# Kernel optimization log

Hardware: AMD Instinct MI355X
Metric: run time of the kernel (lower is better)

Reference implementation:

```python
import jax, jax.numpy as jnp
import numpy as np

CONF_THRES = 0.4
IOU_THRES = 0.45
MAX_WH = 4096.0   # class offset for non-agnostic NMS (torch code: max_wh)
K_PRE = 1024      # candidates kept for the O(K^2) NMS stage (<= max_nms=30000)
MAX_DET = 300     # max detections per image (torch default)
B, N, NC = 16, 25200, 80


def xywh2xyxy(x):
    xy, wh = x[..., :2], x[..., 2:4]
    return jnp.concatenate([xy - wh * 0.5, xy + wh * 0.5], axis=-1)


def box_iou(a, b):
    # a: [K,4], b: [K,4] in xyxy
    area_a = (a[:, 2] - a[:, 0]) * (a[:, 3] - a[:, 1])
    area_b = (b[:, 2] - b[:, 0]) * (b[:, 3] - b[:, 1])
    lt = jnp.maximum(a[:, None, :2], b[None, :, :2])
    rb = jnp.minimum(a[:, None, 2:], b[None, :, 2:])
    inter = jnp.clip(rb - lt, 0.0, None).prod(-1)
    return inter / (area_a[:, None] + area_b[None, :] - inter + 1e-7)


def _nms_single(pred, conf_logit, logit, head):
    # pred [N,85] (decoded, sigmoided), conf_logit [N,5] raw, logit [N,80] raw, head [N]
    xc = pred[:, 4] > CONF_THRES                      # objectness gate
    obj_sig = jax.nn.sigmoid(conf_logit[:, 4:5])      # [N,1]
    log_sig = jax.nn.sigmoid(logit) * obj_sig         # sel_prob == 'objclass'
    cls_scores = pred[:, 5:] * pred[:, 4:5]           # x[:,5:] *= x[:,4:5]
    box = xywh2xyxy(pred[:, :4])                      # [N,4]
    conf = cls_scores.max(axis=1)                     # best class conf
    j = cls_scores.argmax(axis=1).astype(pred.dtype)  # best class id
    valid = xc & (conf > CONF_THRES)
    score = jnp.where(valid, conf, 0.0)
    # top-K candidates (sorted descending) -> fixed-shape NMS
    top_s, top_i = jax.lax.top_k(score, K_PRE)
    valid_k = top_s > 0.0
    boxes_k = box[top_i] + j[top_i, None] * MAX_WH    # per-class box offset (agnostic=False)
    iou = box_iou(boxes_k, boxes_k)                   # [K,K]
    idx = jnp.arange(K_PRE)

    def body(i, keep):
        sup = (iou[i] > IOU_THRES) & (idx > i) & keep[i]
        return keep & ~sup

    keep = jax.lax.fori_loop(0, K_PRE, body, valid_k)
    final_score = jnp.where(keep, top_s, 0.0)
    _, sel = jax.lax.top_k(final_score, MAX_DET)      # first MAX_DET survivors
    gi = top_i[sel]
    m = (final_score[sel] > 0.0).astype(pred.dtype)[:, None]  # validity mask
    det = jnp.concatenate([box[gi], conf[gi, None], j[gi, None]], axis=1)  # [300,6] xyxy,conf,cls
    # pack: det(6) | class logits*obj(80) | obj_conf(1) | classHead(1) | valid(1) -> [300,89]
    return jnp.concatenate(
        [det * m, log_sig[gi] * m, obj_sig[gi] * m, head[gi, None] * m, m], axis=1)


def setup_inputs() -> dict:
    key = jax.random.key(0)
    k1, k2, k3, k4, k5, k6 = jax.random.split(key, 6)
    xy = jax.random.uniform(k1, (B, N, 2), jnp.float32) * 640.0
    wh = 2.0 + jax.random.uniform(k2, (B, N, 2), jnp.float32) * 198.0
    objcls = jax.random.uniform(k3, (B, N, 1 + NC), jnp.float32)
    prediction = jnp.concatenate([xy, wh, objcls], axis=-1)       # [B,N,85]
    pred_conf_logits = jax.random.normal(k4, (B, N, 5), jnp.float32)
    logits = jax.random.normal(k5, (B, N, NC), jnp.float32)
    class_head = jax.random.randint(k6, (B, N), 0, 3).astype(jnp.float32)
    return {"prediction": prediction, "pred_conf_logits": pred_conf_logits,
            "logits": logits, "class_head": class_head}


def reference(prediction, pred_conf_logits, logits, class_head):
    return jax.vmap(_nms_single)(prediction, pred_conf_logits, logits, class_head)
```

## Files before the change

kernel.cpp:

```cpp
#include <hip/hip_runtime.h>
#include <math.h>

#define BATCH 16
#define NN 25200
#define NCLS 80
#define K_PRE 1024
#define MAX_DET 300
#define CONF_T 0.4f
#define IOU_T 0.45f
#define TBIAS 0x3E000000u
#define RROWS 128
#define STHREADS 512
#define CAND_STRIDE 50400

__global__ void __launch_bounds__(STHREADS) score_kernel(
    const float* __restrict__ pred, unsigned long long* __restrict__ keys,
    unsigned* __restrict__ ghist) {
    __shared__ float srow[RROWS * 85];
    __shared__ unsigned lh[1024];

    const int tile = blockIdx.x, b = blockIdx.y, tid = threadIdx.x;
    const int row0 = tile * RROWS;
    int nrows = NN - row0;
    if (nrows > RROWS) nrows = RROWS;

    const float4* g4 = (const float4*)(pred + ((size_t)b * NN + row0) * 85);
    float4* l4 = (float4*)srow;
    const int nf4 = (nrows * 85) >> 2;
    for (int i = tid; i < nf4; i += STHREADS) l4[i] = g4[i];
    lh[tid] = 0u;
    lh[tid + STHREADS] = 0u;
    __syncthreads();

    const int r = tid >> 2, sub = tid & 3;
    float best = 0.0f;
    int bc = sub * 20;
    float obj = 0.0f;
    if (r < nrows) {
        obj = srow[r * 85 + 4];
        if (obj > CONF_T) {
            const float* cp = &srow[r * 85 + 5 + sub * 20];
#pragma unroll
            for (int i = 0; i < 20; ++i) {
                float v = cp[i] * obj;
                if (v > best) { best = v; bc = sub * 20 + i; }
            }
        }
    }
#pragma unroll
    for (int d = 1; d < 4; d <<= 1) {
        float ov = __shfl_xor(best, d);
        int oc = __shfl_xor(bc, d);
        if (ov > best || (ov == best && oc < bc)) { best = ov; bc = oc; }
    }
    if (r < nrows && sub == 0) {
        unsigned t = (obj > CONF_T && best > CONF_T)
                         ? (__float_as_uint(best) - TBIAS) : 0u;
        int n = row0 + r;
        keys[(size_t)b * NN + n] =
            ((unsigned long long)t << 22) |
            ((unsigned long long)(unsigned)(NN - 1 - n) << 7) | (unsigned)bc;
        if (t) atomicAdd(&lh[t >> 15], 1u);
    }
    __syncthreads();
    for (int i = tid; i < 1024; i += STHREADS) {
        unsigned v = lh[i];
        if (v) atomicAdd(&ghist[b * 1024 + i], v);
    }
}

__global__ void __launch_bounds__(1024) topk_kernel(
    const unsigned long long* __restrict__ keys,
    const unsigned* __restrict__ ghist, const float* __restrict__ pred,
    float* __restrict__ ws_f) {
    __shared__ unsigned sA[1024], sB[1024];
    __shared__ unsigned long long skeys[2048];
    __shared__ unsigned sel_d0, sel_cnt;

    const int b = blockIdx.x, tid = threadIdx.x;
    const unsigned long long* bk = keys + (size_t)b * NN;

    unsigned* src = sA;
    unsigned* dst = sB;
    src[tid] = ghist[b * 1024 + tid];
    __syncthreads();
    for (int off = 1; off < 1024; off <<= 1) {
        dst[tid] = src[tid] + ((tid + off < 1024) ? src[tid + off] : 0u);
        __syncthreads();
        unsigned* t2 = src; src = dst; dst = t2;
    }
    unsigned total = src[0];
    unsigned K = total < 1024u ? total : 1024u;
    if (tid == 0) { sel_d0 = 0u; sel_cnt = 0u; }
    skeys[tid] = 0ull;
    skeys[tid + 1024] = 0ull;
    __syncthreads();
    if (total) {
        unsigned geq = src[tid];
        unsigned gt = (tid < 1023) ? src[tid + 1] : 0u;
        if (gt < K && K <= geq) sel_d0 = (unsigned)tid;
    }
    __syncthreads();
    const unsigned d0 = sel_d0;

    for (int base = 0; base < 25600; base += 1024) {
        int i = base + tid;
        if (i < NN) {
            unsigned long long key = bk[i];
            unsigned t = (unsigned)(key >> 22);
            if (t && (t >> 15) >= d0) {
                unsigned p = atomicAdd(&sel_cnt, 1u);
                if (p < 2048u) skeys[p] = key;
            }
        }
    }
    __syncthreads();

    for (unsigned k2 = 2; k2 <= 2048; k2 <<= 1) {
        for (unsigned j = k2 >> 1; j > 0; j >>= 1) {
            unsigned i = ((tid & ~(j - 1)) << 1) | (tid & (j - 1));
            unsigned ixj = i | j;
            unsigned long long a = skeys[i], c = skeys[ixj];
            bool desc = ((i & k2) == 0u);
            if (desc ? (a < c) : (a > c)) { skeys[i] = c; skeys[ixj] = a; }
            __syncthreads();
        }
    }

    unsigned long long key = skeys[tid];
    unsigned t = (unsigned)(key >> 22);
    int n = NN - 1 - (int)((key >> 7) & 32767u);
    float* cbase = ws_f + (size_t)b * CAND_STRIDE;
    float* cx0 = cbase;
    float* cy0 = cbase + 1024;
    float* cx1 = cbase + 2048;
    float* cy1 = cbase + 3072;
    float* carea = cbase + 4096;
    float* cscore = cbase + 5120;
    int* ccls = (int*)(cbase + 6144);
    int* cgi = (int*)(cbase + 7168);
    int* keep = (int*)(cbase + 8192);
    keep[tid] = 0;
    cgi[tid] = n;
    if (t == 0u) {
        ccls[tid] = 255;
    } else {
        const float* row = pred + ((size_t)b * NN + n) * 85;
        float x = row[0], y = row[1], w = row[2], h = row[3];
        float bx0 = x - w * 0.5f, by0 = y - h * 0.5f;
        float bx1 = x + w * 0.5f, by1 = y + h * 0.5f;
        cx0[tid] = bx0; cy0[tid] = by0; cx1[tid] = bx1; cy1[tid] = by1;
        carea[tid] = (bx1 - bx0) * (by1 - by0);
        cscore[tid] = __uint_as_float(t + TBIAS);
        ccls[tid] = (int)(key & 127u);
    }
}

__global__ void __launch_bounds__(64) nms_kernel(float* __restrict__ ws_f) {
    __shared__ int mlist[K_PRE];
    __shared__ float bx0[K_PRE], by0[K_PRE], bx1[K_PRE], by1[K_PRE],
        bar[K_PRE];
    __shared__ unsigned char kf[K_PRE];

    const int b = blockIdx.x / NCLS, c = blockIdx.x % NCLS;
    const int lane = threadIdx.x;
    float* cbase = ws_f + (size_t)b * CAND_STRIDE;
    const float* cx0 = cbase;
    const float* cy0 = cbase + 1024;
    const float* cx1 = cbase + 2048;
    const float* cy1 = cbase + 3072;
    const float* carea = cbase + 4096;
    const int* ccls = (const int*)(cbase + 6144);
    int* keep = (int*)(cbase + 8192);

    int m = 0;
    for (int w = 0; w < K_PRE / 64; ++w) {
        int i = w * 64 + lane;
        bool my = (ccls[i] == c);
        unsigned long long bal = __ballot(my);
        if (my) {
            int pos = __popcll(bal & ((1ull << lane) - 1ull));
            mlist[m + pos] = i;
        }
        m += __popcll(bal);
    }
    for (int j = lane; j < m; j += 64) {
        int i = mlist[j];
        bx0[j] = cx0[i]; by0[j] = cy0[i];
        bx1[j] = cx1[i]; by1[j] = cy1[i];
        bar[j] = carea[i];
        kf[j] = 1;
    }
    __syncthreads();

    for (int i = 0; i < m; ++i) {
        if (kf[i]) {
            float ax0 = bx0[i], ay0 = by0[i], ax1 = bx1[i], ay1 = by1[i];
            float aa = bar[i];
            for (int j = i + 1 + lane; j < m; j += 64) {
                if (kf[j]) {
                    float lx = fmaxf(ax0, bx0[j]);
                    float ly = fmaxf(ay0, by0[j]);
                    float rx = fminf(ax1, bx1[j]);
                    float ry = fminf(ay1, by1[j]);
                    float iw = fmaxf(rx - lx, 0.0f);
                    float ih = fmaxf(ry - ly, 0.0f);
                    float inter = iw * ih;
                    float iou = inter / (aa + bar[j] - inter + 1e-7f);
                    if (iou > IOU_T) kf[j] = 0;
                }
            }
        }
        __syncthreads();
    }
    for (int j = lane; j < m; j += 64)
        if (kf[j]) keep[mlist[j]] = 1;
}

__global__ void __launch_bounds__(1024) output_kernel(
    const float* __restrict__ conf_logits, const float* __restrict__ logits,
    const float* __restrict__ head, const float* __restrict__ ws_f,
    float* __restrict__ out) {
    __shared__ unsigned sA[1024], sB[1024];
    const int b = blockIdx.x, tid = threadIdx.x;
    const float* cbase = ws_f + (size_t)b * CAND_STRIDE;
    const float* cx0 = cbase;
    const float* cy0 = cbase + 1024;
    const float* cx1 = cbase + 2048;
    const float* cy1 = cbase + 3072;
    const float* cscore = cbase + 5120;
    const int* ccls = (const int*)(cbase + 6144);
    const int* cgi = (const int*)(cbase + 7168);
    const int* keep = (const int*)(cbase + 8192);

    int kp = keep[tid];
    unsigned* src = sA;
    unsigned* dst = sB;
    src[tid] = (unsigned)kp;
    __syncthreads();
    for (int off = 1; off < 1024; off <<= 1) {
        dst[tid] = src[tid] + ((tid >= off) ? src[tid - off] : 0u);
        __syncthreads();
        unsigned* t2 = src; src = dst; dst = t2;
    }
    int rank = (int)src[tid] - kp;

    if (kp && rank < MAX_DET) {
        int gi = cgi[tid];
        float* orow = out + ((size_t)b * MAX_DET + rank) * 89;
        orow[0] = cx0[tid]; orow[1] = cy0[tid];
        orow[2] = cx1[tid]; orow[3] = cy1[tid];
        orow[4] = cscore[tid];
        orow[5] = (float)ccls[tid];
        float cl = conf_logits[((size_t)b * NN + gi) * 5 + 4];
        float obj_sig = 1.0f / (1.0f + expf(-cl));
        const float4* lrow4 =
            (const float4*)(logits + ((size_t)b * NN + gi) * NCLS);
#pragma unroll 4
        for (int q = 0; q < 20; ++q) {
            float4 l4 = lrow4[q];
            orow[6 + 4 * q + 0] = obj_sig / (1.0f + expf(-l4.x));
            orow[6 + 4 * q + 1] = obj_sig / (1.0f + expf(-l4.y));
            orow[6 + 4 * q + 2] = obj_sig / (1.0f + expf(-l4.z));
            orow[6 + 4 * q + 3] = obj_sig / (1.0f + expf(-l4.w));
        }
        orow[86] = obj_sig;
        orow[87] = head[(size_t)b * NN + gi];
        orow[88] = 1.0f;
    }
}

extern "C" void kernel_launch(void* const* d_in, const int* in_sizes, int n_in,
                              void* d_out, int out_size, void* d_ws,
                              size_t ws_size, hipStream_t stream) {
    const float* pred        = (const float*)d_in[0];
    const float* conf_logits = (const float*)d_in[1];
    const float* logits      = (const float*)d_in[2];
    const float* head        = (const float*)d_in[3];
    float* out = (float*)d_out;

    char* ws = (char*)d_ws;
    unsigned long long* keys = (unsigned long long*)ws;
    unsigned* ghist = (unsigned*)(ws + (size_t)BATCH * NN * 8);
    float* ws_f = (float*)ws;

    hipMemsetAsync(d_out, 0, (size_t)out_size * sizeof(float), stream);
    hipMemsetAsync(ghist, 0, (size_t)BATCH * 1024 * sizeof(unsigned), stream);

    dim3 sgrid((NN + RROWS - 1) / RROWS, BATCH);
    score_kernel<<<sgrid, STHREADS, 0, stream>>>(pred, keys, ghist);
    topk_kernel<<<BATCH, 1024, 0, stream>>>(keys, ghist, pred, ws_f);
    nms_kernel<<<BATCH * NCLS, 64, 0, stream>>>(ws_f);
    output_kernel<<<BATCH, 1024, 0, stream>>>(conf_logits, logits, head, ws_f,
                                              out);
}
```

Measured before the change: 334.5 us.

## Fuse topk, per-class NMS and output into one per-batch kernel

Merges the top-k selection, per-class NMS and output packing into a single 1024-thread block per image. Candidates stay in shared memory, and each wave handles five classes with wave-level barriers instead of block syncs. The global histogram atomics and both memsets are removed. The histogram is rebuilt by rereading keys, and output zeroing moves in-kernel. The cost is that only 16 blocks run the heavy stages, and per-class lists are capped at 256 entries, which could truncate.

```diff
diff --git a/kernel.cpp b/kernel.cpp
--- a/kernel.cpp
+++ b/kernel.cpp
@@ -11,13 +11,10 @@
 #define TBIAS 0x3E000000u
 #define RROWS 128
 #define STHREADS 512
-#define CAND_STRIDE 50400
 
 __global__ void __launch_bounds__(STHREADS) score_kernel(
-    const float* __restrict__ pred, unsigned long long* __restrict__ keys,
-    unsigned* __restrict__ ghist) {
+    const float* __restrict__ pred, unsigned long long* __restrict__ keys) {
     __shared__ float srow[RROWS * 85];
-    __shared__ unsigned lh[1024];
 
     const int tile = blockIdx.x, b = blockIdx.y, tid = threadIdx.x;
     const int row0 = tile * RROWS;
@@ -28,8 +25,6 @@
     float4* l4 = (float4*)srow;
     const int nf4 = (nrows * 85) >> 2;
     for (int i = tid; i < nf4; i += STHREADS) l4[i] = g4[i];
-    lh[tid] = 0u;
-    lh[tid + STHREADS] = 0u;
     __syncthreads();
 
     const int r = tid >> 2, sub = tid & 3;
@@ -60,30 +55,45 @@
         keys[(size_t)b * NN + n] =
             ((unsigned long long)t << 22) |
             ((unsigned long long)(unsigned)(NN - 1 - n) << 7) | (unsigned)bc;
-        if (t) atomicAdd(&lh[t >> 15], 1u);
-    }
-    __syncthreads();
-    for (int i = tid; i < 1024; i += STHREADS) {
-        unsigned v = lh[i];
-        if (v) atomicAdd(&ghist[b * 1024 + i], v);
     }
 }
 
-__global__ void __launch_bounds__(1024) topk_kernel(
-    const unsigned long long* __restrict__ keys,
-    const unsigned* __restrict__ ghist, const float* __restrict__ pred,
-    float* __restrict__ ws_f) {
+__global__ void __launch_bounds__(1024) fused_kernel(
+    const unsigned long long* __restrict__ keys, const float* __restrict__ pred,
+    const float* __restrict__ conf_logits, const float* __restrict__ logits,
+    const float* __restrict__ head, float* __restrict__ out) {
     __shared__ unsigned sA[1024], sB[1024];
     __shared__ unsigned long long skeys[2048];
+    __shared__ float bx0[K_PRE], by0[K_PRE], bx1[K_PRE], by1[K_PRE],
+        bar[K_PRE];
+    __shared__ short mlist[16 * 256];
+    __shared__ unsigned char kf_s[K_PRE];
     __shared__ unsigned sel_d0, sel_cnt;
+    volatile unsigned char* kf = kf_s;
 
     const int b = blockIdx.x, tid = threadIdx.x;
     const unsigned long long* bk = keys + (size_t)b * NN;
 
+    float* ob = out + (size_t)b * MAX_DET * 89;
+    for (int i = tid; i < MAX_DET * 89; i += 1024) ob[i] = 0.0f;
+
+    sA[tid] = 0u;
+    skeys[tid] = 0ull;
+    skeys[tid + 1024] = 0ull;
+    if (tid == 0) { sel_d0 = 0u; sel_cnt = 0u; }
+    __syncthreads();
+
+    for (int base = 0; base < 25600; base += 1024) {
+        int i = base + tid;
+        if (i < NN) {
+            unsigned t = (unsigned)(bk[i] >> 22);
+            if (t) atomicAdd(&sA[t >> 15], 1u);
+        }
+    }
+    __syncthreads();
+
     unsigned* src = sA;
     unsigned* dst = sB;
-    src[tid] = ghist[b * 1024 + tid];
-    __syncthreads();
     for (int off = 1; off < 1024; off <<= 1) {
         dst[tid] = src[tid] + ((tid + off < 1024) ? src[tid + off] : 0u);
         __syncthreads();
@@ -91,10 +101,6 @@
     }
     unsigned total = src[0];
     unsigned K = total < 1024u ? total : 1024u;
-    if (tid == 0) { sel_d0 = 0u; sel_cnt = 0u; }
-    skeys[tid] = 0ull;
-    skeys[tid + 1024] = 0ull;
-    __syncthreads();
     if (total) {
         unsigned geq = src[tid];
         unsigned gt = (tid < 1023) ? src[tid + 1] : 0u;
@@ -118,7 +124,7 @@
 
     for (unsigned k2 = 2; k2 <= 2048; k2 <<= 1) {
         for (unsigned j = k2 >> 1; j > 0; j >>= 1) {
-            unsigned i = ((tid & ~(j - 1)) << 1) | (tid & (j - 1));
+            unsigned i = (((unsigned)tid & ~(j - 1)) << 1) | ((unsigned)tid & (j - 1));
             unsigned ixj = i | j;
             unsigned long long a = skeys[i], c = skeys[ixj];
             bool desc = ((i & k2) == 0u);
@@ -127,115 +133,67 @@
         }
     }
 
-    unsigned long long key = skeys[tid];
-    unsigned t = (unsigned)(key >> 22);
-    int n = NN - 1 - (int)((key >> 7) & 32767u);
-    float* cbase = ws_f + (size_t)b * CAND_STRIDE;
-    float* cx0 = cbase;
-    float* cy0 = cbase + 1024;
-    float* cx1 = cbase + 2048;
-    float* cy1 = cbase + 3072;
-    float* carea = cbase + 4096;
-    float* cscore = cbase + 5120;
-    int* ccls = (int*)(cbase + 6144);
-    int* cgi = (int*)(cbase + 7168);
-    int* keep = (int*)(cbase + 8192);
-    keep[tid] = 0;
-    cgi[tid] = n;
-    if (t == 0u) {
-        ccls[tid] = 255;
-    } else {
+    unsigned long long mykey = skeys[tid];
+    unsigned t = (unsigned)(mykey >> 22);
+    int n = NN - 1 - (int)((mykey >> 7) & 32767u);
+    if (t) {
         const float* row = pred + ((size_t)b * NN + n) * 85;
         float x = row[0], y = row[1], w = row[2], h = row[3];
-        float bx0 = x - w * 0.5f, by0 = y - h * 0.5f;
-        float bx1 = x + w * 0.5f, by1 = y + h * 0.5f;
-        cx0[tid] = bx0; cy0[tid] = by0; cx1[tid] = bx1; cy1[tid] = by1;
-        carea[tid] = (bx1 - bx0) * (by1 - by0);
-        cscore[tid] = __uint_as_float(t + TBIAS);
-        ccls[tid] = (int)(key & 127u);
-    }
-}
-
-__global__ void __launch_bounds__(64) nms_kernel(float* __restrict__ ws_f) {
-    __shared__ int mlist[K_PRE];
-    __shared__ float bx0[K_PRE], by0[K_PRE], bx1[K_PRE], by1[K_PRE],
-        bar[K_PRE];
-    __shared__ unsigned char kf[K_PRE];
-
-    const int b = blockIdx.x / NCLS, c = blockIdx.x % NCLS;
-    const int lane = threadIdx.x;
-    float* cbase = ws_f + (size_t)b * CAND_STRIDE;
-    const float* cx0 = cbase;
-    const float* cy0 = cbase + 1024;
-    const float* cx1 = cbase + 2048;
-    const float* cy1 = cbase + 3072;
-    const float* carea = cbase + 4096;
-    const int* ccls = (const int*)(cbase + 6144);
-    int* keep = (int*)(cbase + 8192);
-
-    int m = 0;
-    for (int w = 0; w < K_PRE / 64; ++w) {
-        int i = w * 64 + lane;
-        bool my = (ccls[i] == c);
-        unsigned long long bal = __ballot(my);
-        if (my) {
-            int pos = __popcll(bal & ((1ull << lane) - 1ull));
-            mlist[m + pos] = i;
-        }
-        m += __popcll(bal);
-    }
-    for (int j = lane; j < m; j += 64) {
-        int i = mlist[j];
-        bx0[j] = cx0[i]; by0[j] = cy0[i];
-        bx1[j] = cx1[i]; by1[j] = cy1[i];
-        bar[j] = carea[i];
-        kf[j] = 1;
-    }
-    __syncthreads();
-
-    for (int i = 0; i < m; ++i) {
-        if (kf[i]) {
-            float ax0 = bx0[i], ay0 = by0[i], ax1 = bx1[i], ay1 = by1[i];
-            float aa = bar[i];
-            for (int j = i + 1 + lane; j < m; j += 64) {
-                if (kf[j]) {
-                    float lx = fmaxf(ax0, bx0[j]);
-                    float ly = fmaxf(ay0, by0[j]);
-                    float rx = fminf(ax1, bx1[j]);
-                    float ry = fminf(ay1, by1[j]);
-                    float iw = fmaxf(rx - lx, 0.0f);
-                    float ih = fmaxf(ry - ly, 0.0f);
-                    float inter = iw * ih;
-                    float iou = inter / (aa + bar[j] - inter + 1e-7f);
-                    if (iou > IOU_T) kf[j] = 0;
+        float x0 = x - w * 0.5f, y0 = y - h * 0.5f;
+        float x1 = x + w * 0.5f, y1 = y + h * 0.5f;
+        bx0[tid] = x0; by0[tid] = y0; bx1[tid] = x1; by1[tid] = y1;
+        bar[tid] = (x1 - x0) * (y1 - y0);
+        kf_s[tid] = 1;
+    } else {
+        kf_s[tid] = 0;
+    }
+    __syncthreads();
+
+    const int wave = tid >> 6, lane = tid & 63;
+    short* ml = &mlist[wave * 256];
+    for (int q = 0; q < 5; ++q) {
+        int c = wave + 16 * q;
+        int m = 0;
+        for (int chunk = 0; chunk < 16; ++chunk) {
+            int i = chunk * 64 + lane;
+            unsigned long long kk = skeys[i];
+            bool my = ((kk >> 22) != 0ull) && ((int)(kk & 127u) == c);
+            unsigned long long bal = __ballot(my);
+            if (my) {
+                int pos = __popcll(bal & ((1ull << lane) - 1ull));
+                if (m + pos < 256) ml[m + pos] = (short)i;
+            }
+            m += __popcll(bal);
+        }
+        if (m > 256) m = 256;
+        for (int i = 0; i < m - 1; ++i) {
+            __builtin_amdgcn_wave_barrier();
+            int ci = ml[i];
+            if (kf[ci]) {
+                float ax0 = bx0[ci], ay0 = by0[ci];
+                float ax1 = bx1[ci], ay1 = by1[ci];
+                float aa = bar[ci];
+                for (int j = i + 1 + lane; j < m; j += 64) {
+                    int cj = ml[j];
+                    if (kf[cj]) {
+                        float lx = fmaxf(ax0, bx0[cj]);
+                        float ly = fmaxf(ay0, by0[cj]);
+                        float rx = fminf(ax1, bx1[cj]);
+                        float ry = fminf(ay1, by1[cj]);
+                        float iw = fmaxf(rx - lx, 0.0f);
+                        float ih = fmaxf(ry - ly, 0.0f);
+                        float inter = iw * ih;
+                        float iou = inter / (aa + bar[cj] - inter + 1e-7f);
+                        if (iou > IOU_T) kf[cj] = 0;
+                    }
                 }
             }
         }
-        __syncthreads();
-    }
-    for (int j = lane; j < m; j += 64)
-        if (kf[j]) keep[mlist[j]] = 1;
-}
-
-__global__ void __launch_bounds__(1024) output_kernel(
-    const float* __restrict__ conf_logits, const float* __restrict__ logits,
-    const float* __restrict__ head, const float* __restrict__ ws_f,
-    float* __restrict__ out) {
-    __shared__ unsigned sA[1024], sB[1024];
-    const int b = blockIdx.x, tid = threadIdx.x;
-    const float* cbase = ws_f + (size_t)b * CAND_STRIDE;
-    const float* cx0 = cbase;
-    const float* cy0 = cbase + 1024;
-    const float* cx1 = cbase + 2048;
-    const float* cy1 = cbase + 3072;
-    const float* cscore = cbase + 5120;
-    const int* ccls = (const int*)(cbase + 6144);
-    const int* cgi = (const int*)(cbase + 7168);
-    const int* keep = (const int*)(cbase + 8192);
-
-    int kp = keep[tid];
-    unsigned* src = sA;
-    unsigned* dst = sB;
+    }
+    __syncthreads();
+
+    int kp = kf_s[tid] ? 1 : 0;
+    src = sA; dst = sB;
     src[tid] = (unsigned)kp;
     __syncthreads();
     for (int off = 1; off < 1024; off <<= 1) {
@@ -246,26 +204,25 @@
     int rank = (int)src[tid] - kp;
 
     if (kp && rank < MAX_DET) {
-        int gi = cgi[tid];
-        float* orow = out + ((size_t)b * MAX_DET + rank) * 89;
-        orow[0] = cx0[tid]; orow[1] = cy0[tid];
-        orow[2] = cx1[tid]; orow[3] = cy1[tid];
-        orow[4] = cscore[tid];
-        orow[5] = (float)ccls[tid];
-        float cl = conf_logits[((size_t)b * NN + gi) * 5 + 4];
+        float* orow = ob + (size_t)rank * 89;
+        orow[0] = bx0[tid]; orow[1] = by0[tid];
+        orow[2] = bx1[tid]; orow[3] = by1[tid];
+        orow[4] = __uint_as_float(t + TBIAS);
+        orow[5] = (float)(int)(mykey & 127u);
+        float cl = conf_logits[((size_t)b * NN + n) * 5 + 4];
         float obj_sig = 1.0f / (1.0f + expf(-cl));
         const float4* lrow4 =
-            (const float4*)(logits + ((size_t)b * NN + gi) * NCLS);
+            (const float4*)(logits + ((size_t)b * NN + n) * NCLS);
 #pragma unroll 4
         for (int q = 0; q < 20; ++q) {
             float4 l4 = lrow4[q];
-            orow[6 + 4 * q + 0] = obj_sig / (1.0f + expf(-l4.x));
-            orow[6 + 4 * q + 1] = obj_sig / (1.0f + expf(-l4.y));
-            orow[6 + 4 * q + 2] = obj_sig / (1.0f + expf(-l4.z));
-            orow[6 + 4 * q + 3] = obj_sig / (1.0f + expf(-l4.w));
+            orow[6 + 4 * q + 0] = (1.0f / (1.0f + expf(-l4.x))) * obj_sig;
+            orow[6 + 4 * q + 1] = (1.0f / (1.0f + expf(-l4.y))) * obj_sig;
+            orow[6 + 4 * q + 2] = (1.0f / (1.0f + expf(-l4.z))) * obj_sig;
+            orow[6 + 4 * q + 3] = (1.0f / (1.0f + expf(-l4.w))) * obj_sig;
         }
         orow[86] = obj_sig;
-        orow[87] = head[(size_t)b * NN + gi];
+        orow[87] = head[(size_t)b * NN + n];
         orow[88] = 1.0f;
     }
 }
@@ -279,18 +236,10 @@
     const float* head        = (const float*)d_in[3];
     float* out = (float*)d_out;
 
-    char* ws = (char*)d_ws;
-    unsigned long long* keys = (unsigned long long*)ws;
-    unsigned* ghist = (unsigned*)(ws + (size_t)BATCH * NN * 8);
-    float* ws_f = (float*)ws;
-
-    hipMemsetAsync(d_out, 0, (size_t)out_size * sizeof(float), stream);
-    hipMemsetAsync(ghist, 0, (size_t)BATCH * 1024 * sizeof(unsigned), stream);
+    unsigned long long* keys = (unsigned long long*)d_ws;
 
     dim3 sgrid((NN + RROWS - 1) / RROWS, BATCH);
-    score_kernel<<<sgrid, STHREADS, 0, stream>>>(pred, keys, ghist);
-    topk_kernel<<<BATCH, 1024, 0, stream>>>(keys, ghist, pred, ws_f);
-    nms_kernel<<<BATCH * NCLS, 64, 0, stream>>>(ws_f);
-    output_kernel<<<BATCH, 1024, 0, stream>>>(conf_logits, logits, head, ws_f,
-                                              out);
+    score_kernel<<<sgrid, STHREADS, 0, stream>>>(pred, keys);
+    fused_kernel<<<BATCH, 1024, 0, stream>>>(keys, pred, conf_logits, logits,
+                                             head, out);
 }
```

Result: slower. 349.4 us (+4.4%).
